# Performance work log

Measured on AMD Instinct MI355X. Metric: run time of the kernel, lower is better.

Reference implementation:

```python
import jax, jax.numpy as jnp
import numpy as np

D_MODEL = 1024
NUM_HEADS = 16


def _linear(x, W, b):
    # torch nn.Linear: y = x @ W.T + b
    return jnp.einsum('bsd,od->bso', x, W) + b


def _split_heads(x, H):
    B, S, D = x.shape
    return x.reshape(B, S, H, D // H).transpose(0, 2, 1, 3)  # [B,H,S,dk]


def setup_inputs() -> dict:
    key0 = jax.random.key(0)
    ks = jax.random.split(key0, 11)
    B, S, D = 4, 2048, D_MODEL
    w_scale = 1.0 / np.sqrt(D)
    inp = {
        'query': jax.random.normal(ks[0], (B, S, D), jnp.float32),
        'key': jax.random.normal(ks[1], (B, S, D), jnp.float32),
        'value': jax.random.normal(ks[2], (B, S, D), jnp.float32),
        'Wq': jax.random.normal(ks[3], (D, D), jnp.float32) * w_scale,
        'bq': jax.random.normal(ks[4], (D,), jnp.float32) * 0.01,
        'Wk': jax.random.normal(ks[5], (D, D), jnp.float32) * w_scale,
        'bk': jax.random.normal(ks[6], (D,), jnp.float32) * 0.01,
        'Wv': jax.random.normal(ks[7], (D, D), jnp.float32) * w_scale,
        'bv': jax.random.normal(ks[8], (D,), jnp.float32) * 0.01,
        'Wo': jax.random.normal(ks[9], (D, D), jnp.float32) * w_scale,
        'bo': jax.random.normal(ks[10], (D,), jnp.float32) * 0.01,
        'common_prefix_len': 1792,
    }
    return inp


def reference(query, key, value, Wq, bq, Wk, bk, Wv, bv, Wo, bo, common_prefix_len):
    B, S, D = query.shape
    H = NUM_HEADS
    dk = D // H
    P = common_prefix_len
    scale = 1.0 / np.sqrt(dk)

    Q = _split_heads(_linear(query, Wq, bq), H)  # [B,H,S,dk]
    K = _split_heads(_linear(key, Wk, bk), H)
    V = _split_heads(_linear(value, Wv, bv), H)

    # --- prefix: causal self-attention over first P tokens ---
    Qp, Kp, Vp = Q[:, :, :P], K[:, :, :P], V[:, :, :P]
    sp = jnp.einsum('bhld,bhsd->bhls', Qp, Kp) * scale  # [B,H,P,P]
    causal = jnp.tril(jnp.ones((P, P), dtype=bool))
    sp = jnp.where(causal, sp, -jnp.inf)
    prefix_ctx = jnp.einsum('bhls,bhsd->bhld', jax.nn.softmax(sp, axis=-1), Vp)

    # --- candidates: attend to full prefix + own diagonal entry ---
    Qc = Q[:, :, P:]  # [B,H,N,dk]
    N = S - P
    sc = jnp.einsum('bhld,bhsd->bhls', Qc, K) * scale  # [B,H,N,S]
    mask = jnp.concatenate(
        [jnp.ones((N, P), dtype=bool), jnp.eye(N, dtype=bool)], axis=-1)  # [N,S]
    sc = jnp.where(mask, sc, -jnp.inf)
    cand_ctx = jnp.einsum('bhls,bhsd->bhld', jax.nn.softmax(sc, axis=-1), V)

    ctx = jnp.concatenate([prefix_ctx, cand_ctx], axis=2)  # [B,H,S,dk]
    ctx = ctx.transpose(0, 2, 1, 3).reshape(B, S, D)
    return _linear(ctx, Wo, bo)
```

## Files before the change

kernel.cpp:

```cpp
#include <hip/hip_runtime.h>
#include <hip/hip_bf16.h>
#include <stdint.h>
#include <stddef.h>

#define D_M   1024
#define N_H   16
#define D_K   64
#define S_LEN 2048
#define N_B   4
#define P_LEN 1792
#define M_ROWS (N_B*S_LEN)

#define QSCALE 0.1803368801111601f

typedef unsigned short u16;
typedef __bf16  bf16x8 __attribute__((ext_vector_type(8)));
typedef __bf16  bf16x4 __attribute__((ext_vector_type(4)));
typedef __bf16  bf16x2 __attribute__((ext_vector_type(2)));
typedef float   f32x4  __attribute__((ext_vector_type(4)));
typedef float   f32x16 __attribute__((ext_vector_type(16)));
typedef unsigned u32x4 __attribute__((ext_vector_type(4)));

#define MFMA32(a,b,c)   __builtin_amdgcn_mfma_f32_16x16x32_bf16((a),(b),(c),0,0,0)
#define MFMA3216(a,b,c) __builtin_amdgcn_mfma_f32_32x32x16_bf16((a),(b),(c),0,0,0)

__device__ __forceinline__ float ex2(float x){
#if defined(__HIP_DEVICE_COMPILE__) && __has_builtin(__builtin_amdgcn_exp2f)
  return __builtin_amdgcn_exp2f(x);
#else
  return exp2f(x);
#endif
}

#define GLDS16(gp, lp) __builtin_amdgcn_global_load_lds( \
    (__attribute__((address_space(1))) void*)(gp), \
    (__attribute__((address_space(3))) void*)(lp), 16, 0, 0)

__device__ __forceinline__ u16 f2bf(float f){
  unsigned u = __builtin_bit_cast(unsigned, f);
  u += 0x7FFFu + ((u>>16)&1u);
  return (u16)(u>>16);
}

__device__ __forceinline__ unsigned pkbf(float a, float b){
  bf16x2 t; t[0] = (__bf16)a; t[1] = (__bf16)b;
  return __builtin_bit_cast(unsigned, t);
}

__device__ __forceinline__ void plswap(unsigned &x, unsigned &y){
  asm("v_permlane32_swap_b32 %0, %1" : "+v"(x), "+v"(y));
}

__global__ void cvt_bf16(const float* __restrict__ in, u16* __restrict__ out, int n8){
  typedef u16 u16x8 __attribute__((ext_vector_type(8)));
  for (int i = blockIdx.x*blockDim.x + threadIdx.x; i < n8; i += gridDim.x*blockDim.x){
    const float4* p = (const float4*)(in + (size_t)i*8);
    float4 a = p[0], b = p[1];
    u16x8 o;
    o[0]=f2bf(a.x); o[1]=f2bf(a.y); o[2]=f2bf(a.z); o[3]=f2bf(a.w);
    o[4]=f2bf(b.x); o[5]=f2bf(b.y); o[6]=f2bf(b.z); o[7]=f2bf(b.w);
    *(u16x8*)(out + (size_t)i*8) = o;
  }
}

template<int MODE, int SWZ>
__global__ __launch_bounds__(256,3)
void gemm_bt(const u16* __restrict__ A, const u16* __restrict__ Bm,
             const float* __restrict__ bias, void* __restrict__ Cout, float scale)
{
  constexpr int Kd = 1024, N = 1024;
  __shared__ __align__(16) u16 As[128*32];
  __shared__ __align__(16) u16 Bs[128*32];
  const int tid  = threadIdx.x;
  const int wid  = tid >> 6, lane = tid & 63;
  const int rowBase = blockIdx.x * 128, colBase = blockIdx.y * 128;

  const int srow = (wid<<4) + (lane>>2);
  const int scol = (lane&3) << 3;
  const u16* Ag0 = A  + (size_t)(rowBase + srow)*Kd + scol;
  const u16* Ag1 = Ag0 + (size_t)64*Kd;
  const u16* Bg0 = Bm + (size_t)(colBase + srow)*Kd + scol;
  const u16* Bg1 = Bg0 + (size_t)64*Kd;
  u16* AsW0 = As + (wid<<9);
  u16* AsW1 = As + 2048 + (wid<<9);
  u16* BsW0 = Bs + (wid<<9);
  u16* BsW1 = Bs + 2048 + (wid<<9);

  f32x4 acc[4][4] = {};
  const int fr = lane & 15, fk = (lane>>4) << 3;
  const int wr = (wid>>1) << 6, wc = (wid&1) << 6;

  for (int kt = 0; kt < Kd/32; ++kt){
    __syncthreads();
    const int ko = kt*32;
    GLDS16(Ag0+ko, AsW0); GLDS16(Ag1+ko, AsW1);
    GLDS16(Bg0+ko, BsW0); GLDS16(Bg1+ko, BsW1);
    __syncthreads();
    bf16x8 af[4], bf[4];
#pragma unroll
    for (int i=0;i<4;++i) af[i] = *(const bf16x8*)&As[(wr + i*16 + fr)*32 + fk];
#pragma unroll
    for (int i=0;i<4;++i) bf[i] = *(const bf16x8*)&Bs[(wc + i*16 + fr)*32 + fk];
#pragma unroll
    for (int i=0;i<4;++i)
#pragma unroll
      for (int j=0;j<4;++j)
        acc[i][j] = MFMA32(af[i], bf[j], acc[i][j]);
  }

  const int rr0 = (lane>>4) << 2;
#pragma unroll
  for (int i=0;i<4;++i){
#pragma unroll
    for (int j=0;j<4;++j){
      const int gc = colBase + wc + j*16 + fr;
      const float bb = bias[gc];
#pragma unroll
      for (int r=0;r<4;++r){
        const int gr = rowBase + wr + i*16 + rr0 + r;
        const float v = (acc[i][j][r] + bb) * scale;
        if (MODE == 2){
          ((float*)Cout)[(size_t)gr*N + gc] = v;
        } else {
          const int b = gr >> 11, s = gr & 2047;
          const int hh = gc >> 6, k = gc & 63;
          if (MODE == 0){
            const int kk = SWZ ? ((k&7) | ((((k>>3) ^ (s&7)))<<3)) : k;
            ((u16*)Cout)[(((size_t)(b*N_H + hh))*S_LEN + s)*D_K + kk] = f2bf(v);
          } else {
            const int ss = SWZ ? ((s & ~63) | (s&7) | (((((s>>3)&7) ^ (k&7)))<<3)) : s;
            ((u16*)Cout)[(((size_t)(b*N_H + hh))*D_K + k)*S_LEN + ss] = f2bf(v);
          }
        }
      }
    }
  }
}


__device__ __forceinline__ void attn_self(
    const u16* __restrict__ Kb, const u16* __restrict__ Vb,
    const bf16x8* qf, int ks0, int h, int q,
    float& l, f32x16& o0, f32x16& o1)
{
  bf16x8 kr[4];
  {
    const int rr = ks0 + q, sw = rr & 7;
    const u16* kp = Kb + (size_t)rr * D_K;
#pragma unroll
    for (int kb=0;kb<4;++kb)
      kr[kb] = *(const bf16x8*)(kp + (((h + 2*kb) ^ sw) << 3));
  }
  f32x16 s0 = {};
  __builtin_amdgcn_s_setprio(1);
#pragma unroll
  for (int kb=0;kb<4;++kb) s0 = MFMA3216(kr[kb], qf[kb], s0);
  __builtin_amdgcn_s_setprio(0);

  bf16x8 v0[4];
  {
    const int gb = ks0 & ~63, lc0 = (ks0 - gb) >> 3;
    const int sw = q & 7;
#pragma unroll
    for (int db=0;db<2;++db){
      const u16* vp = Vb + (size_t)(32*db + q)*S_LEN + gb;
      v0[2*db]   = *(const bf16x8*)(vp + (((lc0 + h    ) ^ sw) << 3));
      v0[2*db+1] = *(const bf16x8*)(vp + (((lc0 + h + 2) ^ sw) << 3));
    }
  }

  float a[16];
#pragma unroll
  for (int r=0;r<16;++r){
    const int krow = (r&3) + 8*(r>>2) + 4*h;
    float p0 = (krow == q) ? ex2(s0[r]) : 0.f;
    s0[r] = p0; a[r] = p0;
  }
#pragma unroll
  for (int w=8; w>=1; w>>=1)
#pragma unroll
    for (int r=0;r<w;++r) a[r] += a[r+w];
  l += a[0] + __shfl_xor(a[0], 32, 64);

  unsigned w0[8];
#pragma unroll
  for (int i=0;i<8;++i) w0[i] = pkbf(s0[2*i], s0[2*i+1]);
  plswap(w0[0],w0[2]); plswap(w0[1],w0[3]);
  plswap(w0[4],w0[6]); plswap(w0[5],w0[7]);
  bf16x8 p00 = __builtin_bit_cast(bf16x8, (u32x4){w0[0],w0[1],w0[2],w0[3]});
  bf16x8 p01 = __builtin_bit_cast(bf16x8, (u32x4){w0[4],w0[5],w0[6],w0[7]});

  __builtin_amdgcn_s_setprio(1);
  o0 = MFMA3216(v0[0], p00, o0);
  o1 = MFMA3216(v0[2], p00, o1);
  o0 = MFMA3216(v0[1], p01, o0);
  o1 = MFMA3216(v0[3], p01, o1);
  __builtin_amdgcn_s_setprio(0);
}

template<int MASKED>
__device__ __forceinline__ void steplds(
    const u16* __restrict__ Ksb, const u16* __restrict__ Vsb,
    const bf16x8* qf, int ks, int qg, int h, int q,
    float& l, f32x16& o0, f32x16& o1)
{
  bf16x8 kr[8];
#pragma unroll
  for (int s=0;s<2;++s){
    const int rr = 32*s + q, base = rr*64, sw = rr&7;
#pragma unroll
    for (int kb=0;kb<4;++kb)
      kr[4*s+kb] = *(const bf16x8*)&Ksb[base + (((h + 2*kb)^sw)<<3)];
  }
  f32x16 s0 = {}, s1 = {};
  __builtin_amdgcn_s_setprio(1);
#pragma unroll
  for (int kb=0;kb<4;++kb){
    s0 = MFMA3216(kr[kb],   qf[kb], s0);
    s1 = MFMA3216(kr[4+kb], qf[kb], s1);
  }
  __builtin_amdgcn_s_setprio(0);

  bf16x8 v0[4], v1[4];
#pragma unroll
  for (int db=0;db<2;++db){
    const int rd = 32*db + q, base = rd*64, sw = rd&7;
    v0[2*db]   = *(const bf16x8*)&Vsb[base + (((h    )^sw)<<3)];
    v0[2*db+1] = *(const bf16x8*)&Vsb[base + (((h + 2)^sw)<<3)];
    v1[2*db]   = *(const bf16x8*)&Vsb[base + (((h + 4)^sw)<<3)];
    v1[2*db+1] = *(const bf16x8*)&Vsb[base + (((h + 6)^sw)<<3)];
  }

  if (MASKED){
#pragma unroll
    for (int r=0;r<16;++r){
      const int krow = (r&3) + 8*(r>>2) + 4*h;
      if (ks + krow      > qg) s0[r] = -1e30f;
      if (ks + 32 + krow > qg) s1[r] = -1e30f;
    }
  }

  float a[16];
#pragma unroll
  for (int r=0;r<16;++r){
    float p0 = ex2(s0[r]); s0[r] = p0;
    float p1 = ex2(s1[r]); s1[r] = p1;
    a[r] = p0 + p1;
  }
#pragma unroll
  for (int w=8; w>=1; w>>=1)
#pragma unroll
    for (int r=0;r<w;++r) a[r] += a[r+w];
  l += a[0] + __shfl_xor(a[0], 32, 64);

  unsigned w0[8];
#pragma unroll
  for (int i=0;i<8;++i) w0[i] = pkbf(s0[2*i], s0[2*i+1]);
  plswap(w0[0],w0[2]); plswap(w0[1],w0[3]);
  plswap(w0[4],w0[6]); plswap(w0[5],w0[7]);
  bf16x8 p00 = __builtin_bit_cast(bf16x8, (u32x4){w0[0],w0[1],w0[2],w0[3]});
  bf16x8 p01 = __builtin_bit_cast(bf16x8, (u32x4){w0[4],w0[5],w0[6],w0[7]});
  unsigned w1[8];
#pragma unroll
  for (int i=0;i<8;++i) w1[i] = pkbf(s1[2*i], s1[2*i+1]);
  plswap(w1[0],w1[2]); plswap(w1[1],w1[3]);
  plswap(w1[4],w1[6]); plswap(w1[5],w1[7]);
  bf16x8 p10 = __builtin_bit_cast(bf16x8, (u32x4){w1[0],w1[1],w1[2],w1[3]});
  bf16x8 p11 = __builtin_bit_cast(bf16x8, (u32x4){w1[4],w1[5],w1[6],w1[7]});

  __builtin_amdgcn_s_setprio(1);
  o0 = MFMA3216(v0[0], p00, o0);
  o1 = MFMA3216(v0[2], p00, o1);
  o0 = MFMA3216(v0[1], p01, o0);
  o1 = MFMA3216(v0[3], p01, o1);
  o0 = MFMA3216(v1[0], p10, o0);
  o1 = MFMA3216(v1[2], p10, o1);
  o0 = MFMA3216(v1[1], p11, o0);
  o1 = MFMA3216(v1[3], p11, o1);
  __builtin_amdgcn_s_setprio(0);
}

__device__ __forceinline__ void attn_write(
    u16* __restrict__ ctx, int bh, int qg, int h,
    float inv, const f32x16& o0, const f32x16& o1)
{
  const int b = bh >> 4, hd = bh & 15;
  u16* cp = ctx + ((size_t)b*S_LEN + qg)*D_M + hd*D_K;
#pragma unroll
  for (int rg=0; rg<4; ++rg){
    const int d0 = 8*rg + 4*h;
    bf16x4 oa, ob;
#pragma unroll
    for (int e=0;e<4;++e){ oa[e] = (__bf16)(o0[4*rg+e]*inv); ob[e] = (__bf16)(o1[4*rg+e]*inv); }
    *(bf16x4*)(cp + d0)      = oa;
    *(bf16x4*)(cp + 32 + d0) = ob;
  }
}

__global__ __launch_bounds__(128)
void attn_all(const u16* __restrict__ Q, const u16* __restrict__ K,
              const u16* __restrict__ Vt, u16* __restrict__ ctx)
{
  __shared__ __align__(16) u16 Ksm[2][4096];
  __shared__ __align__(16) u16 Vsm[2][4096];

  const int x = blockIdx.x;
  const int type = x >> 6, bh = x & 63;
  const int wid = threadIdx.x >> 6, lane = threadIdx.x & 63;
  const int q = lane & 31, h = lane >> 5;
  const bool iscand = (type < 4);
  const int tt = 31 - type;
  const int qb = iscand ? (P_LEN + (type<<6) + (wid<<5)) : ((tt<<6) + (wid<<5));
  const int nsteps = iscand ? (P_LEN/64) : (tt+1);
  const int qg = qb + q;

  const u16* Kb = K  + (size_t)bh * S_LEN * D_K;
  const u16* Vb = Vt + (size_t)bh * D_K * S_LEN;
  const u16* Qp = Q + ((size_t)bh * S_LEN + qg) * D_K + (h<<3);
  bf16x8 qf[4];
#pragma unroll
  for (int kb=0;kb<4;++kb) qf[kb] = *(const bf16x8*)(Qp + 16*kb);

  float l = 0.f;
  f32x16 o0 = {}, o1 = {};

  const int rl = lane >> 3, cl = (lane & 7) << 3;
  const int rb = wid << 5;

#define STAGE(T, B) do{                                                        \
    const int _ks = (T) << 6;                                                  \
    _Pragma("unroll")                                                          \
    for (int g=0; g<4; ++g){                                                   \
      const int _r = rb + (g<<3);                                              \
      GLDS16(Kb + (size_t)(_ks + _r + rl)*D_K + cl,   &Ksm[B][_r<<6]);         \
      GLDS16(Vb + (size_t)(_r + rl)*S_LEN + _ks + cl, &Vsm[B][_r<<6]);         \
    }                                                                          \
  }while(0)

  STAGE(0, 0);
  __syncthreads();

  for (int t = 0; t < nsteps; ++t){
    if (t+1 < nsteps) STAGE(t+1, (t+1)&1);
    if (!iscand && t == nsteps-1)
      steplds<1>(Ksm[t&1], Vsm[t&1], qf, t<<6, qg, h, q, l, o0, o1);
    else
      steplds<0>(Ksm[t&1], Vsm[t&1], qf, t<<6, qg, h, q, l, o0, o1);
    __syncthreads();
  }
#undef STAGE

  if (iscand)
    attn_self(Kb, Vb, qf, qb, h, q, l, o0, o1);

  attn_write(ctx, bh, qg, h, 1.f/l, o0, o1);
}

extern "C" void kernel_launch(void* const* d_in, const int* in_sizes, int n_in,
                              void* d_out, int out_size, void* d_ws, size_t ws_size,
                              hipStream_t stream)
{
  const float* query = (const float*)d_in[0];
  const float* key   = (const float*)d_in[1];
  const float* value = (const float*)d_in[2];
  const float* Wq = (const float*)d_in[3];
  const float* bq = (const float*)d_in[4];
  const float* Wk = (const float*)d_in[5];
  const float* bk = (const float*)d_in[6];
  const float* Wv = (const float*)d_in[7];
  const float* bv = (const float*)d_in[8];
  const float* Wo = (const float*)d_in[9];
  const float* bo = (const float*)d_in[10];

  if (ws_size < (size_t)(66u<<20)) return;

  char* ws = (char*)d_ws;
  u16* Xb = (u16*)(ws);
  u16* Wb = (u16*)(ws + (16u<<20));
  u16* Qb = (u16*)(ws + (18u<<20));
  u16* Kb = (u16*)(ws + (34u<<20));
  u16* Vb = (u16*)(ws + (50u<<20));
  u16* ctx = Xb;

  const int nX8 = (M_ROWS*D_M)/8, nW8 = (D_M*D_M)/8;
  dim3 gg(M_ROWS/128, D_M/128);

  cvt_bf16<<<2048,256,0,stream>>>(query, Xb, nX8);
  cvt_bf16<<<512, 256,0,stream>>>(Wq,    Wb, nW8);
  gemm_bt<0,0><<<gg,256,0,stream>>>(Xb, Wb, bq, Qb, QSCALE);

  cvt_bf16<<<2048,256,0,stream>>>(key,   Xb, nX8);
  cvt_bf16<<<512, 256,0,stream>>>(Wk,    Wb, nW8);
  gemm_bt<0,1><<<gg,256,0,stream>>>(Xb, Wb, bk, Kb, 1.0f);

  cvt_bf16<<<2048,256,0,stream>>>(value, Xb, nX8);
  cvt_bf16<<<512, 256,0,stream>>>(Wv,    Wb, nW8);
  gemm_bt<1,1><<<gg,256,0,stream>>>(Xb, Wb, bv, Vb, 1.0f);

  attn_all<<<dim3(2048), 128, 0, stream>>>(Qb, Kb, Vb, ctx);

  cvt_bf16<<<512,256,0,stream>>>(Wo, Wb, nW8);
  gemm_bt<2,0><<<gg,256,0,stream>>>(ctx, Wb, bo, (float*)d_out, 1.0f);
}
```

Measured before the change: 200.4 us.

## Fuse fp32 activation conversion into projection GEMM and stream V from global

```diff
diff --git a/kernel.cpp b/kernel.cpp
--- a/kernel.cpp
+++ b/kernel.cpp
@@ -63,9 +63,9 @@
   }
 }
 
-template<int MODE, int SWZ>
-__global__ __launch_bounds__(256,3)
-void gemm_bt(const u16* __restrict__ A, const u16* __restrict__ Bm,
+template<int MODE, int SWZ, int CVT>
+__global__ __launch_bounds__(256,2)
+void gemm_bt(const void* __restrict__ Ain, const u16* __restrict__ Bm,
              const float* __restrict__ bias, void* __restrict__ Cout, float scale)
 {
   constexpr int Kd = 1024, N = 1024;
@@ -77,8 +77,16 @@
 
   const int srow = (wid<<4) + (lane>>2);
   const int scol = (lane&3) << 3;
-  const u16* Ag0 = A  + (size_t)(rowBase + srow)*Kd + scol;
+  const u16* A16 = (const u16*)Ain;
+  const float* A32 = (const float*)Ain;
+
+  const u16* Ag0 = A16 + (size_t)(rowBase + srow)*Kd + scol;
   const u16* Ag1 = Ag0 + (size_t)64*Kd;
+  const int arow  = tid >> 1;
+  const int acol  = (tid & 1) << 4;
+  const float* Af = A32 + (size_t)(rowBase + arow)*Kd + acol;
+  u16* AsD = As + arow*32 + acol;
+
   const u16* Bg0 = Bm + (size_t)(colBase + srow)*Kd + scol;
   const u16* Bg1 = Bg0 + (size_t)64*Kd;
   u16* AsW0 = As + (wid<<9);
@@ -93,7 +101,16 @@
   for (int kt = 0; kt < Kd/32; ++kt){
     __syncthreads();
     const int ko = kt*32;
-    GLDS16(Ag0+ko, AsW0); GLDS16(Ag1+ko, AsW1);
+    if (CVT){
+      const float4* ap = (const float4*)(Af + ko);
+      float4 f0 = ap[0], f1 = ap[1], f2 = ap[2], f3 = ap[3];
+      u32x4 lo = { pkbf(f0.x,f0.y), pkbf(f0.z,f0.w), pkbf(f1.x,f1.y), pkbf(f1.z,f1.w) };
+      u32x4 hi = { pkbf(f2.x,f2.y), pkbf(f2.z,f2.w), pkbf(f3.x,f3.y), pkbf(f3.z,f3.w) };
+      *(u32x4*)(AsD)     = lo;
+      *(u32x4*)(AsD + 8) = hi;
+    } else {
+      GLDS16(Ag0+ko, AsW0); GLDS16(Ag1+ko, AsW1);
+    }
     GLDS16(Bg0+ko, BsW0); GLDS16(Bg1+ko, BsW1);
     __syncthreads();
     bf16x8 af[4], bf[4];
@@ -200,7 +217,7 @@
 
 template<int MASKED>
 __device__ __forceinline__ void steplds(
-    const u16* __restrict__ Ksb, const u16* __restrict__ Vsb,
+    const u16* __restrict__ Ksb, const u16* __restrict__ Vg,
     const bf16x8* qf, int ks, int qg, int h, int q,
     float& l, f32x16& o0, f32x16& o1)
 {
@@ -222,13 +239,16 @@
   __builtin_amdgcn_s_setprio(0);
 
   bf16x8 v0[4], v1[4];
-#pragma unroll
-  for (int db=0;db<2;++db){
-    const int rd = 32*db + q, base = rd*64, sw = rd&7;
-    v0[2*db]   = *(const bf16x8*)&Vsb[base + (((h    )^sw)<<3)];
-    v0[2*db+1] = *(const bf16x8*)&Vsb[base + (((h + 2)^sw)<<3)];
-    v1[2*db]   = *(const bf16x8*)&Vsb[base + (((h + 4)^sw)<<3)];
-    v1[2*db+1] = *(const bf16x8*)&Vsb[base + (((h + 6)^sw)<<3)];
+  {
+    const int sw = q & 7;
+#pragma unroll
+    for (int db=0;db<2;++db){
+      const u16* vp = Vg + (size_t)(32*db + q)*S_LEN + ks;
+      v0[2*db]   = *(const bf16x8*)(vp + (((h    )^sw)<<3));
+      v0[2*db+1] = *(const bf16x8*)(vp + (((h + 2)^sw)<<3));
+      v1[2*db]   = *(const bf16x8*)(vp + (((h + 4)^sw)<<3));
+      v1[2*db+1] = *(const bf16x8*)(vp + (((h + 6)^sw)<<3));
+    }
   }
 
   if (MASKED){
@@ -302,7 +322,6 @@
               const u16* __restrict__ Vt, u16* __restrict__ ctx)
 {
   __shared__ __align__(16) u16 Ksm[2][4096];
-  __shared__ __align__(16) u16 Vsm[2][4096];
 
   const int x = blockIdx.x;
   const int type = x >> 6, bh = x & 63;
@@ -332,21 +351,25 @@
     _Pragma("unroll")                                                          \
     for (int g=0; g<4; ++g){                                                   \
       const int _r = rb + (g<<3);                                              \
-      GLDS16(Kb + (size_t)(_ks + _r + rl)*D_K + cl,   &Ksm[B][_r<<6]);         \
-      GLDS16(Vb + (size_t)(_r + rl)*S_LEN + _ks + cl, &Vsm[B][_r<<6]);         \
+      GLDS16(Kb + (size_t)(_ks + _r + rl)*D_K + cl, &Ksm[B][_r<<6]);           \
     }                                                                          \
   }while(0)
 
   STAGE(0, 0);
-  __syncthreads();
+  if (nsteps > 1) STAGE(1, 1);
 
   for (int t = 0; t < nsteps; ++t){
-    if (t+1 < nsteps) STAGE(t+1, (t+1)&1);
+    if (t+1 < nsteps) asm volatile("s_waitcnt vmcnt(4)" ::: "memory");
+    else              asm volatile("s_waitcnt vmcnt(0)" ::: "memory");
+    __builtin_amdgcn_s_barrier();
+    __builtin_amdgcn_sched_barrier(0);
     if (!iscand && t == nsteps-1)
-      steplds<1>(Ksm[t&1], Vsm[t&1], qf, t<<6, qg, h, q, l, o0, o1);
+      steplds<1>(Ksm[t&1], Vb, qf, t<<6, qg, h, q, l, o0, o1);
     else
-      steplds<0>(Ksm[t&1], Vsm[t&1], qf, t<<6, qg, h, q, l, o0, o1);
-    __syncthreads();
+      steplds<0>(Ksm[t&1], Vb, qf, t<<6, qg, h, q, l, o0, o1);
+    __builtin_amdgcn_sched_barrier(0);
+    __builtin_amdgcn_s_barrier();
+    if (t+2 < nsteps) STAGE(t+2, t&1);
   }
 #undef STAGE
 
@@ -375,30 +398,26 @@
   if (ws_size < (size_t)(66u<<20)) return;
 
   char* ws = (char*)d_ws;
-  u16* Xb = (u16*)(ws);
-  u16* Wb = (u16*)(ws + (16u<<20));
-  u16* Qb = (u16*)(ws + (18u<<20));
-  u16* Kb = (u16*)(ws + (34u<<20));
-  u16* Vb = (u16*)(ws + (50u<<20));
-  u16* ctx = Xb;
-
-  const int nX8 = (M_ROWS*D_M)/8, nW8 = (D_M*D_M)/8;
+  u16* ctx = (u16*)(ws);
+  u16* Wb  = (u16*)(ws + (16u<<20));
+  u16* Qb  = (u16*)(ws + (18u<<20));
+  u16* Kb  = (u16*)(ws + (34u<<20));
+  u16* Vb  = (u16*)(ws + (50u<<20));
+
+  const int nW8 = (D_M*D_M)/8;
   dim3 gg(M_ROWS/128, D_M/128);
 
-  cvt_bf16<<<2048,256,0,stream>>>(query, Xb, nX8);
-  cvt_bf16<<<512, 256,0,stream>>>(Wq,    Wb, nW8);
-  gemm_bt<0,0><<<gg,256,0,stream>>>(Xb, Wb, bq, Qb, QSCALE);
-
-  cvt_bf16<<<2048,256,0,stream>>>(key,   Xb, nX8);
-  cvt_bf16<<<512, 256,0,stream>>>(Wk,    Wb, nW8);
-  gemm_bt<0,1><<<gg,256,0,stream>>>(Xb, Wb, bk, Kb, 1.0f);
-
-  cvt_bf16<<<2048,256,0,stream>>>(value, Xb, nX8);
-  cvt_bf16<<<512, 256,0,stream>>>(Wv,    Wb, nW8);
-  gemm_bt<1,1><<<gg,256,0,stream>>>(Xb, Wb, bv, Vb, 1.0f);
+  cvt_bf16<<<512,256,0,stream>>>(Wq, Wb, nW8);
+  gemm_bt<0,0,1><<<gg,256,0,stream>>>(query, Wb, bq, Qb, QSCALE);
+
+  cvt_bf16<<<512,256,0,stream>>>(Wk, Wb, nW8);
+  gemm_bt<0,1,1><<<gg,256,0,stream>>>(key, Wb, bk, Kb, 1.0f);
+
+  cvt_bf16<<<512,256,0,stream>>>(Wv, Wb, nW8);
+  gemm_bt<1,1,1><<<gg,256,0,stream>>>(value, Wb, bv, Vb, 1.0f);
 
   attn_all<<<dim3(2048), 128, 0, stream>>>(Qb, Kb, Vb, ctx);
 
   cvt_bf16<<<512,256,0,stream>>>(Wo, Wb, nW8);
-  gemm_bt<2,0><<<gg,256,0,stream>>>(ctx, Wb, bo, (float*)d_out, 1.0f);
-}
+  gemm_bt<2,0,0><<<gg,256,0,stream>>>(ctx, Wb, bo, (float*)d_out, 1.0f);
+}
```

Result: slower. 210.4 us (+5.0%).

## Split attention KV range across two wave pairs and read V directly from global

Applied to the files above, without the earlier changes.

```diff
diff --git a/kernel.cpp b/kernel.cpp
--- a/kernel.cpp
+++ b/kernel.cpp
@@ -200,7 +200,7 @@
 
 template<int MASKED>
 __device__ __forceinline__ void steplds(
-    const u16* __restrict__ Ksb, const u16* __restrict__ Vsb,
+    const u16* __restrict__ Ksb, const u16* __restrict__ Vg,
     const bf16x8* qf, int ks, int qg, int h, int q,
     float& l, f32x16& o0, f32x16& o1)
 {
@@ -222,13 +222,16 @@
   __builtin_amdgcn_s_setprio(0);
 
   bf16x8 v0[4], v1[4];
-#pragma unroll
-  for (int db=0;db<2;++db){
-    const int rd = 32*db + q, base = rd*64, sw = rd&7;
-    v0[2*db]   = *(const bf16x8*)&Vsb[base + (((h    )^sw)<<3)];
-    v0[2*db+1] = *(const bf16x8*)&Vsb[base + (((h + 2)^sw)<<3)];
-    v1[2*db]   = *(const bf16x8*)&Vsb[base + (((h + 4)^sw)<<3)];
-    v1[2*db+1] = *(const bf16x8*)&Vsb[base + (((h + 6)^sw)<<3)];
+  {
+    const int sw = q & 7;
+#pragma unroll
+    for (int db=0;db<2;++db){
+      const u16* vp = Vg + (size_t)(32*db + q)*S_LEN + ks;
+      v0[2*db]   = *(const bf16x8*)(vp + (((h    )^sw)<<3));
+      v0[2*db+1] = *(const bf16x8*)(vp + (((h + 2)^sw)<<3));
+      v1[2*db]   = *(const bf16x8*)(vp + (((h + 4)^sw)<<3));
+      v1[2*db+1] = *(const bf16x8*)(vp + (((h + 6)^sw)<<3));
+    }
   }
 
   if (MASKED){
@@ -297,21 +300,33 @@
   }
 }
 
-__global__ __launch_bounds__(128)
+__global__ __launch_bounds__(256)
 void attn_all(const u16* __restrict__ Q, const u16* __restrict__ K,
               const u16* __restrict__ Vt, u16* __restrict__ ctx)
 {
-  __shared__ __align__(16) u16 Ksm[2][4096];
-  __shared__ __align__(16) u16 Vsm[2][4096];
+  __shared__ __align__(16) u16 Ksm[2][2][4096];
 
   const int x = blockIdx.x;
   const int type = x >> 6, bh = x & 63;
   const int wid = threadIdx.x >> 6, lane = threadIdx.x & 63;
   const int q = lane & 31, h = lane >> 5;
+  const int pair = wid >> 1, qs = wid & 1;
   const bool iscand = (type < 4);
   const int tt = 31 - type;
-  const int qb = iscand ? (P_LEN + (type<<6) + (wid<<5)) : ((tt<<6) + (wid<<5));
-  const int nsteps = iscand ? (P_LEN/64) : (tt+1);
+
+  int qb, ks0, n, nmax; bool lastc, doself;
+  if (iscand){
+    qb = P_LEN + (type<<6) + (qs<<5);
+    nmax = 14;
+    if (pair==0){ ks0 = 0;      n = 14; lastc = false; doself = false; }
+    else        { ks0 = 14*64;  n = 14; lastc = false; doself = true;  }
+  } else {
+    qb = (tt<<6) + (qs<<5);
+    const int ntot = tt+1, n0 = (ntot+1)>>1;
+    nmax = n0;
+    if (pair==0){ ks0 = 0;       n = n0;        lastc = (n0==ntot); doself = false; }
+    else        { ks0 = n0<<6;   n = ntot - n0; lastc = (n>0);      doself = false; }
+  }
   const int qg = qb + q;
 
   const u16* Kb = K  + (size_t)bh * S_LEN * D_K;
@@ -325,35 +340,49 @@
   f32x16 o0 = {}, o1 = {};
 
   const int rl = lane >> 3, cl = (lane & 7) << 3;
-  const int rb = wid << 5;
 
 #define STAGE(T, B) do{                                                        \
-    const int _ks = (T) << 6;                                                  \
+    const int _ks = ks0 + ((T) << 6);                                          \
     _Pragma("unroll")                                                          \
     for (int g=0; g<4; ++g){                                                   \
-      const int _r = rb + (g<<3);                                              \
-      GLDS16(Kb + (size_t)(_ks + _r + rl)*D_K + cl,   &Ksm[B][_r<<6]);         \
-      GLDS16(Vb + (size_t)(_r + rl)*S_LEN + _ks + cl, &Vsm[B][_r<<6]);         \
+      const int _r = (qs<<5) + (g<<3);                                         \
+      GLDS16(Kb + (size_t)(_ks + _r + rl)*D_K + cl, &Ksm[pair][B][_r<<6]);     \
     }                                                                          \
   }while(0)
 
-  STAGE(0, 0);
+  if (n > 0) STAGE(0, 0);
   __syncthreads();
 
-  for (int t = 0; t < nsteps; ++t){
-    if (t+1 < nsteps) STAGE(t+1, (t+1)&1);
-    if (!iscand && t == nsteps-1)
-      steplds<1>(Ksm[t&1], Vsm[t&1], qf, t<<6, qg, h, q, l, o0, o1);
-    else
-      steplds<0>(Ksm[t&1], Vsm[t&1], qf, t<<6, qg, h, q, l, o0, o1);
+  for (int t = 0; t < nmax; ++t){
+    if (t+1 < n) STAGE(t+1, (t+1)&1);
+    if (t < n){
+      if (lastc && t == n-1)
+        steplds<1>(Ksm[pair][t&1], Vb, qf, ks0 + (t<<6), qg, h, q, l, o0, o1);
+      else
+        steplds<0>(Ksm[pair][t&1], Vb, qf, ks0 + (t<<6), qg, h, q, l, o0, o1);
+    }
     __syncthreads();
   }
 #undef STAGE
 
-  if (iscand)
+  if (doself)
     attn_self(Kb, Vb, qf, qb, h, q, l, o0, o1);
 
-  attn_write(ctx, bh, qg, h, 1.f/l, o0, o1);
+  float* mbuf = (float*)&Ksm[0][0][0];
+  if (pair == 1){
+    float* p = mbuf + ((qs<<6) + lane)*33;
+#pragma unroll
+    for (int r=0;r<16;++r){ p[r] = o0[r]; p[16+r] = o1[r]; }
+    p[32] = l;
+  }
+  __syncthreads();
+  if (pair == 0){
+    const float* p = mbuf + ((qs<<6) + lane)*33;
+#pragma unroll
+    for (int r=0;r<16;++r){ o0[r] += p[r]; o1[r] += p[16+r]; }
+    l += p[32];
+    attn_write(ctx, bh, qg, h, 1.f/l, o0, o1);
+  }
 }
 
 extern "C" void kernel_launch(void* const* d_in, const int* in_sizes, int n_in,
@@ -397,7 +426,7 @@
   cvt_bf16<<<512, 256,0,stream>>>(Wv,    Wb, nW8);
   gemm_bt<1,1><<<gg,256,0,stream>>>(Xb, Wb, bv, Vb, 1.0f);
 
-  attn_all<<<dim3(2048), 128, 0, stream>>>(Qb, Kb, Vb, ctx);
+  attn_all<<<dim3(2048), 256, 0, stream>>>(Qb, Kb, Vb, ctx);
 
   cvt_bf16<<<512,256,0,stream>>>(Wo, Wb, nW8);
   gemm_bt<2,0><<<gg,256,0,stream>>>(ctx, Wb, bo, (float*)d_out, 1.0f);
```

New measurement: 203.1 us. Within noise of the previous version (+1.3%).
